# Kernel optimization log

Measured on AMD Instinct MI355X. Metric: run time of the kernel, lower is better.

The kernel has to match this reference:

```python
import jax, jax.numpy as jnp
import numpy as np

ANCHORS = np.array([[10.0, 13.0], [16.0, 30.0], [33.0, 23.0]], dtype=np.float32)
IMG_SIZE = 416
NUM_CLASSES = 80
NUM_ANCHORS = 3


def setup_inputs() -> dict:
    key = jax.random.key(0)
    B, G = 64, 52
    C = NUM_ANCHORS * (NUM_CLASSES + 5)  # 255
    x = jax.random.normal(key, (B, C, G, G), dtype=jnp.float32)
    return {"x": x}


def reference(x) -> jnp.ndarray:
    B = x.shape[0]
    G = x.shape[2]
    stride = IMG_SIZE / G
    # [B, A, 5+C, G, G] -> [B, A, G, G, 5+C]
    pred = x.reshape(B, NUM_ANCHORS, NUM_CLASSES + 5, G, G).transpose(0, 1, 3, 4, 2)
    tx = jax.nn.sigmoid(pred[..., 0])
    ty = jax.nn.sigmoid(pred[..., 1])
    tw = pred[..., 2]
    th = pred[..., 3]
    conf = jax.nn.sigmoid(pred[..., 4])
    cls = jax.nn.sigmoid(pred[..., 5:])
    # grid offsets: np.meshgrid(g, g) -> a varies along last axis (cx), b along rows (cy)
    g = jnp.arange(G, dtype=jnp.float32)
    cx = g[None, None, None, :]  # [1,1,1,G]
    cy = g[None, None, :, None]  # [1,1,G,1]
    scaled = jnp.asarray(ANCHORS) / stride  # [A,2]
    aw = scaled[:, 0][None, :, None, None]
    ah = scaled[:, 1][None, :, None, None]
    bbox = jnp.stack(
        [tx + cx, ty + cy, jnp.exp(tw) * aw, jnp.exp(th) * ah], axis=-1
    )  # [B,A,G,G,4]
    bbox_ = bbox.reshape(B, -1, 4) * stride
    conf_ = conf.reshape(B, -1, 1)
    cls_ = cls.reshape(B, -1, NUM_CLASSES)
    return jnp.concatenate([bbox_, conf_, cls_], axis=-1)  # [B, A*G*G, 5+C]
```

## Files before the change

### kernel.cpp

```cpp
#include <hip/hip_runtime.h>


#define GRID 52
#define GG   2704
#define CH   85
#define TS   104
#define NT   26
#define LSTR 105

__global__ __launch_bounds__(256) void det_kernel(const float* __restrict__ in,
                                                  float* __restrict__ out) {
    __shared__ float lds[CH * LSTR];

    const int tile = blockIdx.x;
    const int a    = blockIdx.y;
    const int b    = blockIdx.z;
    const int tid  = threadIdx.x;

    const float4* in4 = (const float4*)(in + ((size_t)b * 255 + (size_t)a * 85) * GG
                                           + (size_t)tile * TS);
    #pragma unroll 4
    for (int l = tid; l < CH * (TS / 4); l += 256) {
        int c  = l / 26;
        int s4 = l - c * 26;
        float4 v = in4[c * 676 + s4];
        float* dst = &lds[c * LSTR + s4 * 4];
        dst[0] = v.x; dst[1] = v.y; dst[2] = v.z; dst[3] = v.w;
    }
    __syncthreads();

    const float AW[3] = {10.f, 16.f, 33.f};
    const float AH[3] = {13.f, 30.f, 23.f};
    const float aw = AW[a], ah = AH[a];

    float* outp = out + ((size_t)b * (3 * GG) + (size_t)a * GG + (size_t)tile * TS) * CH;

    #pragma unroll 4
    for (int o = tid; o < TS * CH; o += 256) {
        int s = o / 85;
        int e = o - s * 85;
        float v = lds[e * LSTR + s];
        float r;
        if (e >= 4) {
            r = 1.f / (1.f + __expf(-v));
        } else if (e == 2) {
            r = __expf(v) * aw;
        } else if (e == 3) {
            r = __expf(v) * ah;
        } else if (e == 4) {
            r = 1.f / (1.f + __expf(-v));
        } else {
            float sig = 1.f / (1.f + __expf(-v));
            int  hi   = (s >= GRID) ? 1 : 0;
            float coord = (e == 0) ? (float)(s - hi * GRID)
                                   : (float)(tile * 2 + hi);
            r = (sig + coord) * 8.0f;
        }
        outp[o] = r;
    }
}

extern "C" void kernel_launch(void* const* d_in, const int* in_sizes, int n_in,
                              void* d_out, int out_size, void* d_ws, size_t ws_size,
                              hipStream_t stream) {
    const float* x = (const float*)d_in[0];
    float* out = (float*)d_out;
    dim3 grid(NT, 3, 64);
    det_kernel<<<grid, 256, 0, stream>>>(x, out);
}
```

Before: 311.0 us.

## Use one-row tiles and a 255-thread stride to hoist per-channel branch logic

Shrinks each block's tile to a single grid row of 52 cells and launches twice as many blocks. Each thread now strides by 255, so it always handles the same channel. The per-element division, modulo and branch selection therefore collapse into loop-invariant scale, sign and addend values, and the output becomes a single exp, a fast reciprocal and an FMA. The cost is one idle thread per block, smaller LDS tiles with more blocks to schedule, and the approximate rcp intrinsic in place of a true division.

```diff
diff --git a/kernel.cpp b/kernel.cpp
--- a/kernel.cpp
+++ b/kernel.cpp
@@ -1,12 +1,10 @@
 #include <hip/hip_runtime.h>
 
 
-#define GRID 52
 #define GG   2704
 #define CH   85
-#define TS   104
-#define NT   26
-#define LSTR 105
+#define TS   52
+#define LSTR 53
 
 __global__ __launch_bounds__(256) void det_kernel(const float* __restrict__ in,
                                                   float* __restrict__ out) {
@@ -19,44 +17,44 @@
 
     const float4* in4 = (const float4*)(in + ((size_t)b * 255 + (size_t)a * 85) * GG
                                            + (size_t)tile * TS);
-    #pragma unroll 4
     for (int l = tid; l < CH * (TS / 4); l += 256) {
-        int c  = l / 26;
-        int s4 = l - c * 26;
+        int c  = l / 13;
+        int s4 = l - c * 13;
         float4 v = in4[c * 676 + s4];
         float* dst = &lds[c * LSTR + s4 * 4];
         dst[0] = v.x; dst[1] = v.y; dst[2] = v.z; dst[3] = v.w;
     }
     __syncthreads();
 
-    const float AW[3] = {10.f, 16.f, 33.f};
-    const float AH[3] = {13.f, 30.f, 23.f};
-    const float aw = AW[a], ah = AH[a];
+    if (tid < 255) {
+        const int e  = tid % 85;
+        const int s0 = tid / 85;
 
-    float* outp = out + ((size_t)b * (3 * GG) + (size_t)a * GG + (size_t)tile * TS) * CH;
+        const float AW[3] = {10.f, 16.f, 33.f};
+        const float AH[3] = {13.f, 30.f, 23.f};
 
-    #pragma unroll 4
-    for (int o = tid; o < TS * CH; o += 256) {
-        int s = o / 85;
-        int e = o - s * 85;
-        float v = lds[e * LSTR + s];
-        float r;
-        if (e >= 4) {
-            r = 1.f / (1.f + __expf(-v));
-        } else if (e == 2) {
-            r = __expf(v) * aw;
-        } else if (e == 3) {
-            r = __expf(v) * ah;
-        } else if (e == 4) {
-            r = 1.f / (1.f + __expf(-v));
-        } else {
-            float sig = 1.f / (1.f + __expf(-v));
-            int  hi   = (s >= GRID) ? 1 : 0;
-            float coord = (e == 0) ? (float)(s - hi * GRID)
-                                   : (float)(tile * 2 + hi);
-            r = (sig + coord) * 8.0f;
+        const bool  isexp = (e == 2) | (e == 3);
+        const float sgn   = isexp ? 1.f : -1.f;
+        float scale;
+        if (e < 2)       scale = 8.f;
+        else if (e == 2) scale = AW[a];
+        else if (e == 3) scale = AH[a];
+        else             scale = 1.f;
+        float addend = (e == 0) ? 8.f * (float)s0
+                     : (e == 1) ? 8.f * (float)tile : 0.f;
+        const float adelta = (e == 0) ? 24.f : 0.f;
+
+        float* op = out + ((size_t)((b * 3 + a) * GG) + (size_t)tile * TS) * CH;
+        int idx = e * LSTR + s0;
+
+        #pragma unroll 2
+        for (int o = tid; o < TS * CH; o += 255, idx += 3) {
+            float v = lds[idx];
+            float t = __expf(sgn * v);
+            float w = isexp ? t : __builtin_amdgcn_rcpf(1.f + t);
+            op[o] = fmaf(scale, w, addend);
+            addend += adelta;
         }
-        outp[o] = r;
     }
 }
 
@@ -65,6 +63,6 @@
                               hipStream_t stream) {
     const float* x = (const float*)d_in[0];
     float* out = (float*)d_out;
-    dim3 grid(NT, 3, 64);
+    dim3 grid(52, 3, 64);
     det_kernel<<<grid, 256, 0, stream>>>(x, out);
 }
```

New measurement: 304.1 us. 1.02x faster.
